# Kernel optimization log

Measured on AMD Instinct MI355X. Metric: run time of the kernel, lower is better.

The kernel has to match this reference:

```python
import jax, jax.numpy as jnp
import numpy as np

N = 100_000   # nodes
E = 1_600_000 # edges
G = 512       # graphs in batch
DIN, DF, DOUT = 78, 32, 128
BN_EPS = 1e-5

def setup_inputs() -> dict:
    key = jax.random.key(0)
    ks = jax.random.split(key, 10)
    s = 0.1
    return {
        "x": jax.random.normal(ks[0], (N, DIN), jnp.float32),
        "edge_index": jax.random.randint(ks[1], (2, E), 0, N, dtype=jnp.int32),
        "batch": jnp.sort(jax.random.randint(ks[2], (N,), 0, G, dtype=jnp.int32)),
        "w1_in": jax.random.normal(ks[3], (DIN, DF), jnp.float32) * s,
        "b1_in": jnp.zeros((DF,), jnp.float32),
        "w1_out": jax.random.normal(ks[4], (DF, DF), jnp.float32) * s,
        "b1_out": jnp.zeros((DF,), jnp.float32),
        "wa": jax.random.normal(ks[5], (4, DF, DF), jnp.float32) * s,
        "ba": jnp.zeros((4, DF), jnp.float32),
        "wb": jax.random.normal(ks[6], (4, DF, DF), jnp.float32) * s,
        "bb": jnp.zeros((4, DF), jnp.float32),
        "gamma": jnp.ones((5, DF), jnp.float32),
        "beta": jnp.zeros((5, DF), jnp.float32),
        "fc_w": jax.random.normal(ks[7], (DF, DOUT), jnp.float32) * s,
        "fc_b": jnp.zeros((DOUT,), jnp.float32),
    }

def _gin_conv(h, src, dst, w1, bv1, w2, bv2):
    # GINConv with eps=0: nn(x + sum_{j in N(i)} x_j)
    agg = jax.ops.segment_sum(h[src], dst, num_segments=N)
    z = h + agg
    return jax.nn.relu(z @ w1 + bv1) @ w2 + bv2

def _bn(h, g, b):
    # BatchNorm1d, training-mode batch statistics (biased variance)
    mu = h.mean(axis=0)
    var = ((h - mu) ** 2).mean(axis=0)
    return g * (h - mu) * jax.lax.rsqrt(var + BN_EPS) + b

def reference(x, edge_index, batch, w1_in, b1_in, w1_out, b1_out,
              wa, ba, wb, bb, gamma, beta, fc_w, fc_b):
    src, dst = edge_index[0], edge_index[1]
    h = _bn(jax.nn.relu(_gin_conv(x, src, dst, w1_in, b1_in, w1_out, b1_out)), gamma[0], beta[0])
    for i in range(4):  # conv2..conv5 (identical shapes)
        h = _bn(jax.nn.relu(_gin_conv(h, src, dst, wa[i], ba[i], wb[i], bb[i])), gamma[i + 1], beta[i + 1])
    pooled = jax.ops.segment_sum(h, batch, num_segments=G)  # global_add_pool -> [G, DF]
    out = jax.nn.relu(pooled @ fc_w + fc_b)
    # dropout omitted (deterministic reference / eval semantics)
    return out
```

## Files before the change

### kernel.cpp

```cpp
#include <hip/hip_runtime.h>
#include <hip/hip_bf16.h>

#define NN 100000
#define EE 1600000
#define GG 512
#define DIN 78
#define DF 32
#define DOUT 128
#define BN_EPS 1e-5f

#define NBLK_NODE 3125

#define BSH 9
#define NBUCK 196
#define SCB 256
#define EPB (EE / SCB)

__global__ __launch_bounds__(256) void k_bhist(const int* __restrict__ dst, int* __restrict__ hist_g) {
    __shared__ int hist[NBUCK];
    int tid = threadIdx.x, blk = blockIdx.x;
    if (tid < NBUCK) hist[tid] = 0;
    __syncthreads();
    int start = blk * EPB, end = start + EPB;
    for (int i = start + tid; i < end; i += 256) atomicAdd(&hist[dst[i] >> BSH], 1);
    __syncthreads();
    if (tid < NBUCK) hist_g[tid * SCB + blk] = hist[tid];
}

__global__ __launch_bounds__(256) void k_bscan(int* __restrict__ hist_g, int* __restrict__ bbase) {
    __shared__ int tot[256];
    int t = threadIdx.x;
    int total = 0;
    if (t < NBUCK)
        for (int blk = 0; blk < SCB; ++blk) total += hist_g[t * SCB + blk];
    tot[t] = (t < NBUCK) ? total : 0;
    __syncthreads();
    for (int off = 1; off < 256; off <<= 1) {
        int u = (t >= off) ? tot[t - off] : 0;
        __syncthreads();
        tot[t] += u;
        __syncthreads();
    }
    int excl = tot[t] - total;
    if (t < NBUCK) {
        bbase[t] = excl;
        int run = excl;
        for (int blk = 0; blk < SCB; ++blk) {
            int h = hist_g[t * SCB + blk];
            hist_g[t * SCB + blk] = run;
            run += h;
        }
    }
    if (t == 0) bbase[NBUCK] = EE;
}

__global__ __launch_bounds__(256) void k_bscatter(const int* __restrict__ src, const int* __restrict__ dst,
                                                  const int* __restrict__ hist_g, int2* __restrict__ pairs) {
    __shared__ int base_l[NBUCK];
    __shared__ int cnt[NBUCK];
    int tid = threadIdx.x, blk = blockIdx.x;
    if (tid < NBUCK) { base_l[tid] = hist_g[tid * SCB + blk]; cnt[tid] = 0; }
    __syncthreads();
    int start = blk * EPB, end = start + EPB;
    for (int i = start + tid; i < end; i += 256) {
        int d = dst[i], s = src[i];
        int b = d >> BSH;
        int rk = atomicAdd(&cnt[b], 1);
        pairs[base_l[b] + rk] = make_int2(s, d);
    }
}

__global__ __launch_bounds__(256) void k_bfill(const int2* __restrict__ pairs, const int* __restrict__ bbase,
                                               int* __restrict__ row_ptr, int* __restrict__ col) {
    __shared__ int cnt[512];
    __shared__ int excl[512];
    __shared__ int ps[256];
    int tid = threadIdx.x, b = blockIdx.x;
    int base = bbase[b];
    int cntb = bbase[b + 1] - base;
    int nbase = b << BSH;
    int nloc = NN - nbase; if (nloc > 512) nloc = 512;
    cnt[tid] = 0; cnt[tid + 256] = 0;
    __syncthreads();
    for (int i = tid; i < cntb; i += 256) atomicAdd(&cnt[pairs[base + i].y - nbase], 1);
    __syncthreads();
    int a0 = cnt[2 * tid], a1 = cnt[2 * tid + 1];
    ps[tid] = a0 + a1;
    __syncthreads();
    for (int off = 1; off < 256; off <<= 1) {
        int u = (tid >= off) ? ps[tid - off] : 0;
        __syncthreads();
        ps[tid] += u;
        __syncthreads();
    }
    int pexcl = ps[tid] - (a0 + a1);
    excl[2 * tid] = pexcl;
    excl[2 * tid + 1] = pexcl + a0;
    __syncthreads();
    for (int i = tid; i < nloc; i += 256) row_ptr[nbase + i] = base + excl[i];
    if (b == 0 && tid == 0) row_ptr[NN] = EE;
    __syncthreads();
    for (int i = tid; i < cntb; i += 256) {
        int2 pr = pairs[base + i];
        int lp = atomicAdd(&excl[pr.y - nbase], 1);
        col[base + lp] = pr.x;
    }
}

__global__ __launch_bounds__(256) void k_proj_first(const float* __restrict__ x,
                                                    const float* __restrict__ w1,
                                                    float* __restrict__ p) {
    __shared__ float w[DIN][DF];
    __shared__ float hx[32][DIN];
    int tid = threadIdx.x;
    for (int i = tid; i < DIN * DF; i += 256) w[i >> 5][i & 31] = w1[i];
    int base = blockIdx.x * 32;
    for (int i = tid; i < 32 * DIN; i += 256) hx[i / DIN][i % DIN] = x[base * DIN + i];
    __syncthreads();
    int j = tid & 31;
    #pragma unroll
    for (int it = 0; it < 4; ++it) {
        int rown = (tid >> 5) + 8 * it;
        float acc = 0.f;
        #pragma unroll
        for (int k = 0; k < DIN; ++k) acc += hx[rown][k] * w[k][j];
        p[(base + rown) * DF + j] = acc;
    }
}

__global__ __launch_bounds__(256) void k_proj_hidden(const float* __restrict__ r,
                                                     const float* __restrict__ w1_,
                                                     const float* __restrict__ statsL,
                                                     const float* __restrict__ gamma,
                                                     const float* __restrict__ beta,
                                                     float* __restrict__ p) {
    __shared__ float w[DF][DF];
    __shared__ float h[32][DF + 1];
    int tid = threadIdx.x;
    for (int i = tid; i < DF * DF; i += 256) w[i >> 5][i & 31] = w1_[i];
    int grp = tid >> 3, c = tid & 7;
    int node = blockIdx.x * 32 + grp;
    const float invN = 1.0f / (float)NN;
    float4 s1v = ((const float4*)statsL)[c];
    float4 s2v = ((const float4*)(statsL + DF))[c];
    float4 gv  = ((const float4*)gamma)[c];
    float4 bv  = ((const float4*)beta)[c];
    float4 rv  = ((const float4*)r)[node * 8 + c];
    float mux = s1v.x * invN, muy = s1v.y * invN, muz = s1v.z * invN, muw = s1v.w * invN;
    float ivx = rsqrtf(s2v.x * invN - mux * mux + BN_EPS);
    float ivy = rsqrtf(s2v.y * invN - muy * muy + BN_EPS);
    float ivz = rsqrtf(s2v.z * invN - muz * muz + BN_EPS);
    float ivw = rsqrtf(s2v.w * invN - muw * muw + BN_EPS);
    h[grp][4 * c + 0] = gv.x * (rv.x - mux) * ivx + bv.x;
    h[grp][4 * c + 1] = gv.y * (rv.y - muy) * ivy + bv.y;
    h[grp][4 * c + 2] = gv.z * (rv.z - muz) * ivz + bv.z;
    h[grp][4 * c + 3] = gv.w * (rv.w - muw) * ivw + bv.w;
    __syncthreads();
    int j = tid & 31;
    #pragma unroll
    for (int it = 0; it < 4; ++it) {
        int rown = (tid >> 5) + 8 * it;
        float acc = 0.f;
        #pragma unroll
        for (int k = 0; k < DF; ++k) acc += h[rown][k] * w[k][j];
        p[(blockIdx.x * 32 + rown) * DF + j] = acc;
    }
}

__global__ __launch_bounds__(256) void k_agg(const float* __restrict__ p,
                                             const int* __restrict__ row_ptr,
                                             const int* __restrict__ col,
                                             const float* __restrict__ b1,
                                             const float* __restrict__ w2_,
                                             const float* __restrict__ b2,
                                             float* __restrict__ r,
                                             float* __restrict__ statsL) {
    __shared__ float w[DF][DF];
    __shared__ float a[32][DF + 1];
    __shared__ float red[4][2][DF];
    int tid = threadIdx.x;
    for (int i = tid; i < DF * DF; i += 256) w[i >> 5][i & 31] = w2_[i];
    int grp = tid >> 3, c = tid & 7;
    int node = blockIdx.x * 32 + grp;
    const float4* p4 = (const float4*)p;
    float4 acc = p4[node * 8 + c];
    int e0 = row_ptr[node], e1 = row_ptr[node + 1];
    for (int e = e0; e < e1; ++e) {
        int srcn = col[e];
        float4 v = p4[srcn * 8 + c];
        acc.x += v.x; acc.y += v.y; acc.z += v.z; acc.w += v.w;
    }
    float4 b1v = ((const float4*)b1)[c];
    a[grp][4 * c + 0] = fmaxf(acc.x + b1v.x, 0.f);
    a[grp][4 * c + 1] = fmaxf(acc.y + b1v.y, 0.f);
    a[grp][4 * c + 2] = fmaxf(acc.z + b1v.z, 0.f);
    a[grp][4 * c + 3] = fmaxf(acc.w + b1v.w, 0.f);
    __syncthreads();
    int j = tid & 31;
    float b2j = b2[j];
    float s1 = 0.f, s2 = 0.f;
    #pragma unroll
    for (int it = 0; it < 4; ++it) {
        int rown = (tid >> 5) + 8 * it;
        float accm = b2j;
        #pragma unroll
        for (int k = 0; k < DF; ++k) accm += a[rown][k] * w[k][j];
        float rv = fmaxf(accm, 0.f);
        r[(blockIdx.x * 32 + rown) * DF + j] = rv;
        s1 += rv;
        s2 += rv * rv;
    }
    s1 += __shfl_down(s1, 32);
    s2 += __shfl_down(s2, 32);
    int wave = tid >> 6, lane = tid & 63;
    if (lane < 32) { red[wave][0][j] = s1; red[wave][1][j] = s2; }
    __syncthreads();
    if (tid < 32) {
        float t1 = red[0][0][j] + red[1][0][j] + red[2][0][j] + red[3][0][j];
        float t2 = red[0][1][j] + red[1][1][j] + red[2][1][j] + red[3][1][j];
        atomicAdd(&statsL[j], t1);
        atomicAdd(&statsL[DF + j], t2);
    }
}

__global__ __launch_bounds__(256) void k_pool(const float* __restrict__ r,
                                              const float* __restrict__ statsL,
                                              const float* __restrict__ gamma,
                                              const float* __restrict__ beta,
                                              const int* __restrict__ batch,
                                              float* __restrict__ pooled) {
    int t = blockIdx.x * 256 + threadIdx.x;
    int nodeBase = (t >> 5) * 8;
    if (nodeBase >= NN) return;
    int j = t & 31;
    const float invN = 1.0f / (float)NN;
    float mu = statsL[j] * invN;
    float inv = rsqrtf(statsL[DF + j] * invN - mu * mu + BN_EPS);
    float gj = gamma[j], bj = beta[j];
    float accp = 0.f;
    int curg = batch[nodeBase];
    #pragma unroll
    for (int k = 0; k < 8; ++k) {
        int n = nodeBase + k;
        int g = batch[n];
        float val = gj * (r[n * DF + j] - mu) * inv + bj;
        if (g != curg) { atomicAdd(&pooled[curg * DF + j], accp); accp = 0.f; curg = g; }
        accp += val;
    }
    atomicAdd(&pooled[curg * DF + j], accp);
}

__global__ __launch_bounds__(128) void k_fc(const float* __restrict__ pooled,
                                            const float* __restrict__ fc_w,
                                            const float* __restrict__ fc_b,
                                            float* __restrict__ out) {
    __shared__ float pl[DF];
    int g = blockIdx.x, j = threadIdx.x;
    if (j < DF) pl[j] = pooled[g * DF + j];
    __syncthreads();
    float acc = fc_b[j];
    #pragma unroll
    for (int k = 0; k < DF; ++k) acc += pl[k] * fc_w[k * DOUT + j];
    out[g * DOUT + j] = fmaxf(acc, 0.f);
}

extern "C" void kernel_launch(void* const* d_in, const int* in_sizes, int n_in,
                              void* d_out, int out_size, void* d_ws, size_t ws_size,
                              hipStream_t stream) {
    const float* x      = (const float*)d_in[0];
    const int*   eidx   = (const int*)d_in[1];
    const int*   batch  = (const int*)d_in[2];
    const float* w1_in  = (const float*)d_in[3];
    const float* b1_in  = (const float*)d_in[4];
    const float* w1_out = (const float*)d_in[5];
    const float* b1_out = (const float*)d_in[6];
    const float* wa     = (const float*)d_in[7];
    const float* ba     = (const float*)d_in[8];
    const float* wb     = (const float*)d_in[9];
    const float* bb     = (const float*)d_in[10];
    const float* gamma  = (const float*)d_in[11];
    const float* beta   = (const float*)d_in[12];
    const float* fc_w   = (const float*)d_in[13];
    const float* fc_b   = (const float*)d_in[14];
    float* out = (float*)d_out;

    const int* esrc = eidx;
    const int* edst = eidx + EE;

    float* W = (float*)d_ws;
    float* p       = W;
    float* r       = p + (size_t)NN * DF;
    float* pooled  = r + (size_t)NN * DF;
    float* stats   = pooled + (size_t)GG * DF;
    int* row_ptr = (int*)(stats + 5 * 64);
    int* col     = row_ptr + (NN + 1);
    int* hist_g  = col + EE;
    int* bbase   = hist_g + NBUCK * SCB;
    int2* pairs  = (int2*)p;

    k_bhist<<<SCB, 256, 0, stream>>>(edst, hist_g);
    k_bscan<<<1, 256, 0, stream>>>(hist_g, bbase);
    k_bscatter<<<SCB, 256, 0, stream>>>(esrc, edst, hist_g, pairs);
    k_bfill<<<NBUCK, 256, 0, stream>>>(pairs, bbase, row_ptr, col);

    hipMemsetAsync(stats, 0, sizeof(float) * 5 * 64, stream);

    k_proj_first<<<NBLK_NODE, 256, 0, stream>>>(x, w1_in, p);
    k_agg<<<NBLK_NODE, 256, 0, stream>>>(p, row_ptr, col, b1_in, w1_out, b1_out, r, stats);

    for (int i = 1; i < 5; ++i) {
        const float* w1_ = wa + (size_t)(i - 1) * DF * DF;
        const float* b1_ = ba + (size_t)(i - 1) * DF;
        const float* w2_ = wb + (size_t)(i - 1) * DF * DF;
        const float* b2_ = bb + (size_t)(i - 1) * DF;
        const float* g_  = gamma + (size_t)(i - 1) * DF;
        const float* be_ = beta + (size_t)(i - 1) * DF;
        k_proj_hidden<<<NBLK_NODE, 256, 0, stream>>>(r, w1_, stats + (i - 1) * 64, g_, be_, p);
        k_agg<<<NBLK_NODE, 256, 0, stream>>>(p, row_ptr, col, b1_, w2_, b2_, r, stats + i * 64);
    }

    hipMemsetAsync(pooled, 0, sizeof(float) * GG * DF, stream);
    k_pool<<<((NN / 8) * 32 + 255) / 256, 256, 0, stream>>>(r, stats + 4 * 64, gamma + 4 * DF,
                                                            beta + 4 * DF, batch, pooled);
    k_fc<<<GG, 128, 0, stream>>>(pooled, fc_w, fc_b, out);
}
```

Measured before the change: 835.4 us.

## Pack edge pairs into single ints and balance aggregation with LDS atomics

```diff
diff --git a/kernel.cpp b/kernel.cpp
--- a/kernel.cpp
+++ b/kernel.cpp
@@ -55,7 +55,7 @@
 }
 
 __global__ __launch_bounds__(256) void k_bscatter(const int* __restrict__ src, const int* __restrict__ dst,
-                                                  const int* __restrict__ hist_g, int2* __restrict__ pairs) {
+                                                  const int* __restrict__ hist_g, int* __restrict__ pairs) {
     __shared__ int base_l[NBUCK];
     __shared__ int cnt[NBUCK];
     int tid = threadIdx.x, blk = blockIdx.x;
@@ -66,11 +66,11 @@
         int d = dst[i], s = src[i];
         int b = d >> BSH;
         int rk = atomicAdd(&cnt[b], 1);
-        pairs[base_l[b] + rk] = make_int2(s, d);
-    }
-}
-
-__global__ __launch_bounds__(256) void k_bfill(const int2* __restrict__ pairs, const int* __restrict__ bbase,
+        pairs[base_l[b] + rk] = s | ((d & 511) << 17);
+    }
+}
+
+__global__ __launch_bounds__(256) void k_bfill(const int* __restrict__ pairs, const int* __restrict__ bbase,
                                                int* __restrict__ row_ptr, int* __restrict__ col) {
     __shared__ int cnt[512];
     __shared__ int excl[512];
@@ -82,7 +82,7 @@
     int nloc = NN - nbase; if (nloc > 512) nloc = 512;
     cnt[tid] = 0; cnt[tid + 256] = 0;
     __syncthreads();
-    for (int i = tid; i < cntb; i += 256) atomicAdd(&cnt[pairs[base + i].y - nbase], 1);
+    for (int i = tid; i < cntb; i += 256) atomicAdd(&cnt[(unsigned)pairs[base + i] >> 17], 1);
     __syncthreads();
     int a0 = cnt[2 * tid], a1 = cnt[2 * tid + 1];
     ps[tid] = a0 + a1;
@@ -101,9 +101,11 @@
     if (b == 0 && tid == 0) row_ptr[NN] = EE;
     __syncthreads();
     for (int i = tid; i < cntb; i += 256) {
-        int2 pr = pairs[base + i];
-        int lp = atomicAdd(&excl[pr.y - nbase], 1);
-        col[base + lp] = pr.x;
+        int v = pairs[base + i];
+        int dloc = (unsigned)v >> 17;
+        int s = v & 0x1FFFF;
+        int lp = atomicAdd(&excl[dloc], 1);
+        col[base + lp] = s | ((dloc & 31) << 25);
     }
 }
 
@@ -181,20 +183,32 @@
     int tid = threadIdx.x;
     for (int i = tid; i < DF * DF; i += 256) w[i >> 5][i & 31] = w2_[i];
     int grp = tid >> 3, c = tid & 7;
-    int node = blockIdx.x * 32 + grp;
+    int base = blockIdx.x * 32;
+    int node = base + grp;
     const float4* p4 = (const float4*)p;
-    float4 acc = p4[node * 8 + c];
-    int e0 = row_ptr[node], e1 = row_ptr[node + 1];
-    for (int e = e0; e < e1; ++e) {
-        int srcn = col[e];
-        float4 v = p4[srcn * 8 + c];
-        acc.x += v.x; acc.y += v.y; acc.z += v.z; acc.w += v.w;
-    }
+    float4 self = p4[node * 8 + c];
     float4 b1v = ((const float4*)b1)[c];
-    a[grp][4 * c + 0] = fmaxf(acc.x + b1v.x, 0.f);
-    a[grp][4 * c + 1] = fmaxf(acc.y + b1v.y, 0.f);
-    a[grp][4 * c + 2] = fmaxf(acc.z + b1v.z, 0.f);
-    a[grp][4 * c + 3] = fmaxf(acc.w + b1v.w, 0.f);
+    a[grp][4 * c + 0] = self.x + b1v.x;
+    a[grp][4 * c + 1] = self.y + b1v.y;
+    a[grp][4 * c + 2] = self.z + b1v.z;
+    a[grp][4 * c + 3] = self.w + b1v.w;
+    __syncthreads();
+    int e0 = row_ptr[base], e1 = row_ptr[base + 32];
+    for (int e = e0 + grp; e < e1; e += 32) {
+        int v = col[e];
+        int srcn = v & 0x01FFFFFF;
+        int loc = ((unsigned)v >> 25) & 31;
+        float4 val = p4[srcn * 8 + c];
+        atomicAdd(&a[loc][4 * c + 0], val.x);
+        atomicAdd(&a[loc][4 * c + 1], val.y);
+        atomicAdd(&a[loc][4 * c + 2], val.z);
+        atomicAdd(&a[loc][4 * c + 3], val.w);
+    }
+    __syncthreads();
+    a[grp][4 * c + 0] = fmaxf(a[grp][4 * c + 0], 0.f);
+    a[grp][4 * c + 1] = fmaxf(a[grp][4 * c + 1], 0.f);
+    a[grp][4 * c + 2] = fmaxf(a[grp][4 * c + 2], 0.f);
+    a[grp][4 * c + 3] = fmaxf(a[grp][4 * c + 3], 0.f);
     __syncthreads();
     int j = tid & 31;
     float b2j = b2[j];
@@ -206,7 +220,7 @@
         #pragma unroll
         for (int k = 0; k < DF; ++k) accm += a[rown][k] * w[k][j];
         float rv = fmaxf(accm, 0.f);
-        r[(blockIdx.x * 32 + rown) * DF + j] = rv;
+        r[(base + rown) * DF + j] = rv;
         s1 += rv;
         s2 += rv * rv;
     }
@@ -296,7 +310,7 @@
     int* col     = row_ptr + (NN + 1);
     int* hist_g  = col + EE;
     int* bbase   = hist_g + NBUCK * SCB;
-    int2* pairs  = (int2*)p;
+    int* pairs   = (int*)p;
 
     k_bhist<<<SCB, 256, 0, stream>>>(edst, hist_g);
     k_bscan<<<1, 256, 0, stream>>>(hist_g, bbase);
```

Result: slower. 1.741 ms (+108.4%).
